# Kernel tuning notes

Measured on AMD Instinct MI355X. Metric: run time of the kernel, lower is better.

## Reference

```python
import jax, jax.numpy as jnp
import numpy as np

NUM_TOKS = 16384
TOK_DIM = 256
B, S = 4, 2048


def setup_inputs() -> dict:
    key = jax.random.key(0)
    k1, k2 = jax.random.split(key)
    h = jax.random.normal(k1, (B, S, TOK_DIM), dtype=jnp.float32)
    w = jax.random.normal(k2, (NUM_TOKS, TOK_DIM), dtype=jnp.float32)
    # module normalizes the codebook rows at init
    w = w / jnp.linalg.norm(w, axis=-1, keepdims=True)
    return {"h": h, "weight": w}


def reference(h, weight):
    # Euclidean distance from each h vector to every codebook row:
    # ||h - w||_2 = sqrt(||h||^2 - 2 h.w + ||w||^2)  (GEMM reformulation of
    # the original broadcast-subtract + norm, same math)
    h2 = jnp.sum(h * h, axis=-1, keepdims=True)          # (B, S, 1)
    w2 = jnp.sum(weight * weight, axis=-1)               # (V,)
    cross = jnp.einsum('bsd,vd->bsv', h, weight)         # (B, S, V)
    sq = jnp.maximum(h2 - 2.0 * cross + w2, 0.0)
    return jnp.sqrt(sq)                                  # (B, S, V) distances (logits semantics)
```

## Files before the change

### kernel.cpp

```cpp
#include <hip/hip_runtime.h>
#include <hip/hip_bf16.h>

static constexpr int M_ = 8192;
static constexpr int N_ = 16384;
static constexpr int K_ = 256;
static constexpr int BM = 128, BN = 128;

typedef __attribute__((ext_vector_type(4))) float f32x4;
typedef __attribute__((ext_vector_type(8))) short bf16x8;

__device__ __forceinline__ ushort f2bf(float f) {
  __hip_bfloat16 b = __float2bfloat16(f);
  return __builtin_bit_cast(ushort, b);
}

__global__ __launch_bounds__(256) void cast_rows_k(
    const float* __restrict__ in, ushort* __restrict__ outb,
    float* __restrict__ sq)
{
  const int row  = blockIdx.x * 4 + (threadIdx.x >> 6);
  const int lane = threadIdx.x & 63;
  const float4 v = reinterpret_cast<const float4*>(in)[(size_t)row * 64 + lane];
  ushort4 o;
  o.x = f2bf(v.x); o.y = f2bf(v.y); o.z = f2bf(v.z); o.w = f2bf(v.w);
  reinterpret_cast<ushort4*>(outb)[(size_t)row * 64 + lane] = o;
  float s = v.x * v.x + v.y * v.y + v.z * v.z + v.w * v.w;
  #pragma unroll
  for (int off = 32; off > 0; off >>= 1) s += __shfl_down(s, off, 64);
  if (lane == 0) sq[row] = s;
}

__global__ __launch_bounds__(256) void dist_gemm_k(
    const ushort* __restrict__ A,
    const ushort* __restrict__ Bm,
    const float* __restrict__ h2,
    const float* __restrict__ w2,
    float* __restrict__ C)
{
  const int lane = threadIdx.x & 63;
  const int wid  = threadIdx.x >> 6;

  const int nwg = gridDim.x;
  const int cpx = nwg >> 3;
  const int bid = (blockIdx.x & 7) * cpx + (blockIdx.x >> 3);

  const int nbn  = N_ / BN;
  const int brow = (bid / nbn) * BM;
  const int bcol = (bid % nbn) * BN;

  const int wrow = (wid >> 1) * 64;
  const int wcol = (wid & 1) * 64;

  const int rl = lane & 15;
  const int kq = (lane >> 4) * 8;
  const ushort* Ab = A  + (size_t)(brow + wrow + rl) * K_ + kq;
  const ushort* Bb = Bm + (size_t)(bcol + wcol + rl) * K_ + kq;

  f32x4 acc[4][4] = {};
  bf16x8 a0[4], b0[4], a1[4], b1[4];

  #pragma unroll
  for (int i = 0; i < 4; ++i) {
    a0[i] = *reinterpret_cast<const bf16x8*>(Ab + (size_t)i * 16 * K_);
    b0[i] = *reinterpret_cast<const bf16x8*>(Bb + (size_t)i * 16 * K_);
  }

  #pragma unroll
  for (int kk = 0; kk < 8; ++kk) {
    const bf16x8* ac = (kk & 1) ? a1 : a0;
    const bf16x8* bc = (kk & 1) ? b1 : b0;
    bf16x8* an = (kk & 1) ? a0 : a1;
    bf16x8* bn = (kk & 1) ? b0 : b1;
    if (kk < 7) {
      const int ko = (kk + 1) * 32;
      #pragma unroll
      for (int i = 0; i < 4; ++i) {
        an[i] = *reinterpret_cast<const bf16x8*>(Ab + (size_t)i * 16 * K_ + ko);
        bn[i] = *reinterpret_cast<const bf16x8*>(Bb + (size_t)i * 16 * K_ + ko);
      }
    }
    #pragma unroll
    for (int i = 0; i < 4; ++i)
      #pragma unroll
      for (int j = 0; j < 4; ++j)
        acc[i][j] = __builtin_amdgcn_mfma_f32_16x16x32_bf16(
            ac[i], bc[j], acc[i][j], 0, 0, 0);
  }

  const int cl   = lane & 15;
  const int row0 = brow + wrow + ((lane >> 4) << 2);
  const int col0 = bcol + wcol;
  float h2v[16];
  #pragma unroll
  for (int i = 0; i < 4; ++i)
    #pragma unroll
    for (int r = 0; r < 4; ++r)
      h2v[i * 4 + r] = h2[row0 + i * 16 + r];

  #pragma unroll
  for (int j = 0; j < 4; ++j) {
    const int col  = col0 + j * 16 + cl;
    const float wc = w2[col];
    #pragma unroll
    for (int i = 0; i < 4; ++i) {
      const int row = row0 + i * 16;
      #pragma unroll
      for (int r = 0; r < 4; ++r) {
        const float v = h2v[i * 4 + r] - 2.0f * acc[i][j][r] + wc;
        __builtin_nontemporal_store(sqrtf(fmaxf(v, 0.0f)),
                                    &C[(size_t)(row + r) * N_ + col]);
      }
    }
  }
}

__global__ void naive_dist_k(const float* __restrict__ h,
                             const float* __restrict__ w,
                             float* __restrict__ C)
{
  const size_t idx = (size_t)blockIdx.x * 256 + threadIdx.x;
  const int m = (int)(idx / N_);
  const int n = (int)(idx % N_);
  const float* hr = h + (size_t)m * K_;
  const float* wr = w + (size_t)n * K_;
  float dot = 0.f, hh = 0.f, ww = 0.f;
  for (int k = 0; k < K_; ++k) {
    const float a = hr[k], b = wr[k];
    dot += a * b; hh += a * a; ww += b * b;
  }
  C[idx] = sqrtf(fmaxf(hh - 2.0f * dot + ww, 0.0f));
}

extern "C" void kernel_launch(void* const* d_in, const int* in_sizes, int n_in,
                              void* d_out, int out_size, void* d_ws, size_t ws_size,
                              hipStream_t stream) {
  const float* h = (const float*)d_in[0];
  const float* w = (const float*)d_in[1];
  float* out = (float*)d_out;

  const size_t need = (size_t)M_ * K_ * 2 + (size_t)N_ * K_ * 2
                    + (size_t)M_ * 4 + (size_t)N_ * 4;
  if (ws_size < need) {
    naive_dist_k<<<(int)(((size_t)M_ * N_) / 256), 256, 0, stream>>>(h, w, out);
    return;
  }

  ushort* hb = (ushort*)d_ws;
  ushort* wb = hb + (size_t)M_ * K_;
  float*  s1 = (float*)(wb + (size_t)N_ * K_);
  float*  s2 = s1 + M_;

  cast_rows_k<<<M_ / 4, 256, 0, stream>>>(h, hb, s1);
  cast_rows_k<<<N_ / 4, 256, 0, stream>>>(w, wb, s2);
  dist_gemm_k<<<(M_ / BM) * (N_ / BN), 256, 0, stream>>>(hb, wb, s1, s2, out);
}
```

Before: 715.9 us.

## Persist A tile in registers and loop blocks over N chunks

Each workgroup now holds its full 128xK slice of h in registers and iterates over 16 column chunks of a 2048-wide N span, with a grid of 512 blocks instead of 8192. B fragments are double-buffered across chunk boundaries, so the next chunk's first slice is prefetched during the last MFMA step. The aim is to cut repeated A loads and per-block launch and prologue overhead. In exchange it raises register pressure (launch_bounds 256,2, A array of 32 bf16x8), may reduce parallelism and overlap of stores with compute, and replaces the nontemporal output stores with plain stores.

```diff
diff --git a/kernel.cpp b/kernel.cpp
--- a/kernel.cpp
+++ b/kernel.cpp
@@ -5,6 +5,10 @@
 static constexpr int N_ = 16384;
 static constexpr int K_ = 256;
 static constexpr int BM = 128, BN = 128;
+static constexpr int NG = 8;
+static constexpr int NSPAN  = N_ / NG;
+static constexpr int CHUNKS = NSPAN / BN;
+static constexpr int STRIPES = M_ / BM;
 
 typedef __attribute__((ext_vector_type(4))) float f32x4;
 typedef __attribute__((ext_vector_type(8))) short bf16x8;
@@ -30,7 +34,7 @@
   if (lane == 0) sq[row] = s;
 }
 
-__global__ __launch_bounds__(256) void dist_gemm_k(
+__global__ __launch_bounds__(256, 2) void dist_gemm_k(
     const ushort* __restrict__ A,
     const ushort* __restrict__ Bm,
     const float* __restrict__ h2,
@@ -40,56 +44,29 @@
   const int lane = threadIdx.x & 63;
   const int wid  = threadIdx.x >> 6;
 
-  const int nwg = gridDim.x;
-  const int cpx = nwg >> 3;
-  const int bid = (blockIdx.x & 7) * cpx + (blockIdx.x >> 3);
-
-  const int nbn  = N_ / BN;
-  const int brow = (bid / nbn) * BM;
-  const int bcol = (bid % nbn) * BN;
+  const int g = blockIdx.x & (NG - 1);
+  const int s = blockIdx.x >> 3;
+  const int brow  = s * BM;
+  const int ncol0 = g * NSPAN;
 
   const int wrow = (wid >> 1) * 64;
   const int wcol = (wid & 1) * 64;
-
   const int rl = lane & 15;
   const int kq = (lane >> 4) * 8;
-  const ushort* Ab = A  + (size_t)(brow + wrow + rl) * K_ + kq;
-  const ushort* Bb = Bm + (size_t)(bcol + wcol + rl) * K_ + kq;
 
-  f32x4 acc[4][4] = {};
-  bf16x8 a0[4], b0[4], a1[4], b1[4];
-
-  #pragma unroll
-  for (int i = 0; i < 4; ++i) {
-    a0[i] = *reinterpret_cast<const bf16x8*>(Ab + (size_t)i * 16 * K_);
-    b0[i] = *reinterpret_cast<const bf16x8*>(Bb + (size_t)i * 16 * K_);
-  }
-
-  #pragma unroll
-  for (int kk = 0; kk < 8; ++kk) {
-    const bf16x8* ac = (kk & 1) ? a1 : a0;
-    const bf16x8* bc = (kk & 1) ? b1 : b0;
-    bf16x8* an = (kk & 1) ? a0 : a1;
-    bf16x8* bn = (kk & 1) ? b0 : b1;
-    if (kk < 7) {
-      const int ko = (kk + 1) * 32;
+  bf16x8 a[8][4];
+  {
+    const ushort* Ab = A + (size_t)(brow + wrow + rl) * K_ + kq;
+    #pragma unroll
+    for (int kk = 0; kk < 8; ++kk)
       #pragma unroll
-      for (int i = 0; i < 4; ++i) {
-        an[i] = *reinterpret_cast<const bf16x8*>(Ab + (size_t)i * 16 * K_ + ko);
-        bn[i] = *reinterpret_cast<const bf16x8*>(Bb + (size_t)i * 16 * K_ + ko);
-      }
-    }
-    #pragma unroll
-    for (int i = 0; i < 4; ++i)
-      #pragma unroll
-      for (int j = 0; j < 4; ++j)
-        acc[i][j] = __builtin_amdgcn_mfma_f32_16x16x32_bf16(
-            ac[i], bc[j], acc[i][j], 0, 0, 0);
+      for (int i = 0; i < 4; ++i)
+        a[kk][i] = *reinterpret_cast<const bf16x8*>(
+            Ab + (size_t)i * 16 * K_ + kk * 32);
   }
 
   const int cl   = lane & 15;
   const int row0 = brow + wrow + ((lane >> 4) << 2);
-  const int col0 = bcol + wcol;
   float h2v[16];
   #pragma unroll
   for (int i = 0; i < 4; ++i)
@@ -97,18 +74,53 @@
     for (int r = 0; r < 4; ++r)
       h2v[i * 4 + r] = h2[row0 + i * 16 + r];
 
+  const ushort* Bw = Bm + (size_t)(ncol0 + wcol + rl) * K_ + kq;
+
+  bf16x8 b0[4], b1[4];
   #pragma unroll
-  for (int j = 0; j < 4; ++j) {
-    const int col  = col0 + j * 16 + cl;
-    const float wc = w2[col];
+  for (int j = 0; j < 4; ++j)
+    b0[j] = *reinterpret_cast<const bf16x8*>(Bw + (size_t)j * 16 * K_);
+
+  for (int c = 0; c < CHUNKS; ++c) {
+    const ushort* Bc = Bw + (size_t)c * BN * K_;
+    f32x4 acc[4][4] = {};
     #pragma unroll
-    for (int i = 0; i < 4; ++i) {
-      const int row = row0 + i * 16;
+    for (int kk = 0; kk < 8; ++kk) {
+      const bf16x8* cur = (kk & 1) ? b1 : b0;
+      bf16x8*       nxt = (kk & 1) ? b0 : b1;
+      if (kk < 7) {
+        const int ko = (kk + 1) * 32;
+        #pragma unroll
+        for (int j = 0; j < 4; ++j)
+          nxt[j] = *reinterpret_cast<const bf16x8*>(
+              Bc + (size_t)j * 16 * K_ + ko);
+      } else if (c + 1 < CHUNKS) {
+        const ushort* Bn = Bw + (size_t)(c + 1) * BN * K_;
+        #pragma unroll
+        for (int j = 0; j < 4; ++j)
+          nxt[j] = *reinterpret_cast<const bf16x8*>(Bn + (size_t)j * 16 * K_);
+      }
       #pragma unroll
-      for (int r = 0; r < 4; ++r) {
-        const float v = h2v[i * 4 + r] - 2.0f * acc[i][j][r] + wc;
-        __builtin_nontemporal_store(sqrtf(fmaxf(v, 0.0f)),
-                                    &C[(size_t)(row + r) * N_ + col]);
+      for (int i = 0; i < 4; ++i)
+        #pragma unroll
+        for (int j = 0; j < 4; ++j)
+          acc[i][j] = __builtin_amdgcn_mfma_f32_16x16x32_bf16(
+              a[kk][i], cur[j], acc[i][j], 0, 0, 0);
+    }
+
+    const int col0 = ncol0 + c * BN + wcol;
+    #pragma unroll
+    for (int j = 0; j < 4; ++j) {
+      const int col  = col0 + j * 16 + cl;
+      const float wc = w2[col];
+      #pragma unroll
+      for (int i = 0; i < 4; ++i) {
+        const int row = row0 + i * 16;
+        #pragma unroll
+        for (int r = 0; r < 4; ++r) {
+          const float v = h2v[i * 4 + r] - 2.0f * acc[i][j][r] + wc;
+          C[(size_t)(row + r) * N_ + col] = sqrtf(fmaxf(v, 0.0f));
+        }
       }
     }
   }
@@ -152,5 +164,5 @@
 
   cast_rows_k<<<M_ / 4, 256, 0, stream>>>(h, hb, s1);
   cast_rows_k<<<N_ / 4, 256, 0, stream>>>(w, wb, s2);
-  dist_gemm_k<<<(M_ / BM) * (N_ / BN), 256, 0, stream>>>(hb, wb, s1, s2, out);
+  dist_gemm_k<<<STRIPES * NG, 256, 0, stream>>>(hb, wb, s1, s2, out);
 }
```

Result: slower. 759.7 us (+6.1%).
